# Performance work log

Hardware: AMD Instinct MI355X
Metric: run time of the kernel (lower is better)

The kernel has to match this reference:

```python
import jax, jax.numpy as jnp
from jax import lax
import numpy as np

B, T, C, L, K, LS = 128, 64, 6625, 25, 6, 25
ALPHA, SMOOTH_TAIL, BLANK = 0.1, 0.01, 0


def setup_inputs() -> dict:
    key = jax.random.key(0)
    k1, k2, k3, k4, k5 = jax.random.split(key, 5)
    preds = jax.random.normal(k1, (B, T, C), jnp.float32)
    text = jax.random.randint(k2, (B, L), 1, C)            # labels avoid blank=0
    length = jax.random.randint(k3, (B,), 10, L + 1)       # master target lengths
    preds_size = jnp.full((B,), T, jnp.int32)              # full time length per sample
    smooth_text = jax.random.randint(k4, (B, K, LS), 1, C)
    smooth_length = jax.random.randint(k5, (B, K), 5, LS + 1)
    return dict(preds=preds, text=text, preds_size=preds_size, length=length,
                smooth_text=smooth_text, smooth_length=smooth_length)


def ctc_nll(log_probs, sample_idx, targets, input_lens, target_lens):
    """Batched CTC negative log likelihood (torch.nn.CTCLoss math, zero_infinity).
    log_probs: [T, Bsrc, C] log-softmax; sample_idx: [N] -> Bsrc (lets N targets
    share logits without materializing [T, N, C]); targets: [N, Lmax]."""
    Tt = log_probs.shape[0]
    N, Lt = targets.shape
    S = 2 * Lt + 1
    NEG = jnp.float32(-1e30)
    ext = jnp.full((N, S), BLANK, dtype=targets.dtype).at[:, 1::2].set(targets)
    ext_m2 = jnp.pad(ext[:, :-2], ((0, 0), (2, 0)), constant_values=BLANK)
    allow_skip = (ext != BLANK) & (ext != ext_m2)          # [N, S]

    def frame(lp_t):                                        # [Bsrc,C] -> [N,S]
        return jnp.take_along_axis(lp_t[sample_idx], ext, axis=1)

    lp0 = frame(log_probs[0])
    alpha = jnp.full((N, S), NEG).at[:, 0].set(lp0[:, 0]).at[:, 1].set(lp0[:, 1])

    def step(alpha, xs):
        t, lp_t = xs
        s1 = jnp.pad(alpha[:, :-1], ((0, 0), (1, 0)), constant_values=NEG)
        s2 = jnp.where(allow_skip,
                       jnp.pad(alpha[:, :-2], ((0, 0), (2, 0)), constant_values=NEG), NEG)
        m = jnp.maximum(alpha, jnp.maximum(s1, s2))
        tot = m + jnp.log(jnp.exp(alpha - m) + jnp.exp(s1 - m) + jnp.exp(s2 - m))
        new = tot + frame(lp_t)
        return jnp.where((t < input_lens)[:, None], new, alpha), None

    alpha, _ = lax.scan(step, alpha, (jnp.arange(1, Tt), log_probs[1:]))
    il = (2 * target_lens)[:, None]                         # final blank position
    a_blank = jnp.take_along_axis(alpha, il, axis=1)[:, 0]
    a_char = jnp.take_along_axis(alpha, jnp.maximum(il - 1, 0), axis=1)[:, 0]
    nll = -jnp.logaddexp(a_blank, a_char)
    return jnp.where(nll > 1e29, 0.0, nll)                  # zero_infinity


def _confidence_beam1(lp):
    """CTC prefix beam search with beam_size=1 on one sample. lp: [T, C] log-probs.
    Returns length-normalized prefix probability as the confidence score."""
    Cc = lp.shape[1]
    NEG = jnp.float32(-1e30)
    cs = jnp.arange(Cc)

    def step(state, lp_t):
        lpb, lpnb, last = state
        tot = jnp.logaddexp(lpb, lpnb)
        new_pb = tot + lp_t[BLANK]
        rep = jnp.where(last >= 0, lpnb + lp_t[jnp.maximum(last, 0)], NEG)
        keep = jnp.logaddexp(new_pb, rep)                   # keep same prefix
        ext = jnp.where(cs == last, lpb, tot) + lp_t        # extend by char c
        ext = ext.at[BLANK].set(NEG)
        best_c = jnp.argmax(ext)
        best_ext = ext[best_c]
        take_ext = best_ext > keep
        return (jnp.where(take_ext, NEG, new_pb),
                jnp.where(take_ext, best_ext, rep),
                jnp.where(take_ext, best_c.astype(jnp.int32), last)), None

    init = (jnp.float32(0.0), NEG, jnp.int32(-1))
    (lpb, lpnb, _), _ = lax.scan(step, init, lp)
    score = jnp.logaddexp(lpb, lpnb)
    return jnp.exp(score / lp.shape[0])


def reference(preds, text, preds_size, length, smooth_text, smooth_length):
    lp = jax.nn.log_softmax(preds, axis=2)                  # [B, T, C]
    lp_tbc = jnp.transpose(lp, (1, 0, 2))                   # [T, B, C]
    conf = lax.stop_gradient(jax.vmap(_confidence_beam1)(lp))  # no_grad block

    # master CTC loss (reduction='mean': nll / target_len, then batch mean)
    nll_m = ctc_nll(lp_tbc, jnp.arange(B), text, preds_size, length)
    loss_master = jnp.mean(nll_m / length.astype(lp.dtype))

    # smoothing CTC losses: K hypotheses per sample share that sample's logits
    idx_s = jnp.repeat(jnp.arange(B), K)
    nll_s = ctc_nll(lp_tbc, idx_s, smooth_text.reshape(B * K, LS),
                    jnp.full((B * K,), T, jnp.int32), smooth_length.reshape(B * K))
    loss_cal = jnp.mean((nll_s / smooth_length.reshape(-1).astype(lp.dtype)).reshape(B, K), axis=1)

    ranking = SMOOTH_TAIL + (1.0 - SMOOTH_TAIL) * (1.0 - conf) ** 2
    return loss_master + jnp.mean(ALPHA * ranking * loss_cal)
```

## Files before the change

kernel.cpp:

```cpp
#include <hip/hip_runtime.h>
#include <cstddef>

#define BB   128
#define TT   64
#define CC   6625
#define LL   25
#define KK   6
#define LSS  25
#define SS   51
#define NEG  (-1e30f)
#define FNEG (-3.4e38f)
#define PIVOT 16.0f

#define NCTC       (BB + BB * KK)
#define CTC_BLOCKS (NCTC / 4)

__device__ __forceinline__ float lae(float a, float b) {
    float m = fmaxf(a, b);
    float n = fminf(a, b);
    return m + __logf(1.0f + __expf(n - m));
}

__global__ __launch_bounds__(256) void row_stats_k(
    const float* __restrict__ preds,
    float* __restrict__ lse_t, float* __restrict__ t1v, float* __restrict__ t2v,
    int* __restrict__ t1i, int* __restrict__ t2i, float* __restrict__ cal)
{
    int r = blockIdx.x;
    int tid = threadIdx.x;
    if (r == 0 && tid < BB) cal[tid] = 0.0f;

    const float* row = preds + (size_t)r * CC;
    float s = 0.0f;
    float v1 = FNEG, v2 = FNEG;
    int   i1 = 0x7fffffff, i2 = 0x7fffffff;

    auto upd = [&](float x, int c) {
        s += __expf(x - PIVOT);
        if (c >= 1) {
            if (x > v1)      { v2 = v1; i2 = i1; v1 = x; i1 = c; }
            else if (x > v2) { v2 = x; i2 = c; }
        }
    };

    int h = (4 - (r & 3)) & 3;
    if (tid < h) upd(row[tid], tid);
    const float4* vp = (const float4*)(row + h);
    int nv = (CC - h) >> 2;
    for (int i = tid; i < nv; i += 256) {
        float4 x = vp[i];
        int c = h + (i << 2);
        upd(x.x, c); upd(x.y, c + 1); upd(x.z, c + 2); upd(x.w, c + 3);
    }
    int tail0 = h + (nv << 2);
    if (tid < CC - tail0) upd(row[tail0 + tid], tail0 + tid);

    for (int off = 32; off > 0; off >>= 1) {
        s += __shfl_xor(s, off);
        float w1 = __shfl_xor(v1, off); int j1 = __shfl_xor(i1, off);
        float w2 = __shfl_xor(v2, off); int j2 = __shfl_xor(i2, off);
        bool b1 = (w1 > v1) || (w1 == v1 && j1 < i1);
        if (b1) {
            bool b2 = (v1 > w2) || (v1 == w2 && i1 < j2);
            v2 = b2 ? v1 : w2; i2 = b2 ? i1 : j2;
            v1 = w1; i1 = j1;
        } else {
            bool b2 = (w1 > v2) || (w1 == v2 && j1 < i2);
            if (b2) { v2 = w1; i2 = j1; }
        }
    }

    __shared__ float ss_[4], sv1[4], sv2[4];
    __shared__ int   si1[4], si2[4];
    int wave = tid >> 6, lane = tid & 63;
    if (lane == 0) { ss_[wave] = s; sv1[wave] = v1; si1[wave] = i1; sv2[wave] = v2; si2[wave] = i2; }
    __syncthreads();
    if (tid == 0) {
        for (int w = 1; w < 4; ++w) {
            s += ss_[w];
            float w1 = sv1[w]; int j1 = si1[w]; float w2 = sv2[w]; int j2 = si2[w];
            bool b1 = (w1 > v1) || (w1 == v1 && j1 < i1);
            if (b1) {
                bool b2 = (v1 > w2) || (v1 == w2 && i1 < j2);
                v2 = b2 ? v1 : w2; i2 = b2 ? i1 : j2;
                v1 = w1; i1 = j1;
            } else {
                bool b2 = (w1 > v2) || (w1 == v2 && j1 < i2);
                if (b2) { v2 = w1; i2 = j1; }
            }
        }
        int b = r >> 6, t = r & 63;
        int tr = t * BB + b;
        lse_t[tr] = PIVOT + __logf(s);
        t1v[tr] = v1; t1i[tr] = i1;
        t2v[tr] = v2; t2i[tr] = i2;
    }
}

__global__ __launch_bounds__(256) void ctc_beam_k(
    const float* __restrict__ preds, const float* __restrict__ lse_t,
    const float* __restrict__ t1v, const float* __restrict__ t2v,
    const int* __restrict__ t1i, const int* __restrict__ t2i,
    const int* __restrict__ text, const int* __restrict__ length,
    const int* __restrict__ preds_size,
    const int* __restrict__ smooth_text, const int* __restrict__ smooth_length,
    float* __restrict__ nllm, float* __restrict__ cal, float* __restrict__ ranking)
{
    if (blockIdx.x == CTC_BLOCKS) {
        int b = threadIdx.x;
        if (b >= BB) return;
        const float* pb = preds + (size_t)b * TT * CC;
        float lpb = 0.0f, lpnb = NEG;
        int last = -1;
        float pf0[4];
        #pragma unroll
        for (int i = 0; i < 4; ++i) pf0[i] = pb[(size_t)i * CC];
        float lplast_raw = 0.0f;
        for (int t = 0; t < TT; ++t) {
            int tr = t * BB + b;
            float lse = lse_t[tr];
            float w1 = t1v[tr]; int j1 = t1i[tr];
            float w2 = t2v[tr]; int j2 = t2i[tr];
            float lp0 = pf0[t & 3] - lse;
            if (t + 4 < TT) pf0[t & 3] = pb[(size_t)(t + 4) * CC];
            float lplast = (last >= 0) ? (lplast_raw - lse) : NEG;
            float tot = lae(lpb, lpnb);
            float new_pb = tot + lp0;
            float rep = (last >= 0) ? (lpnb + lplast) : NEG;
            float keep = lae(new_pb, rep);
            float best_ext; int best_c;
            if (j1 == last) {
                float eA = lpb + (w1 - lse);
                float eB = tot + (w2 - lse);
                if (eA > eB || (eA == eB && last < j2)) { best_ext = eA; best_c = last; }
                else                                    { best_ext = eB; best_c = j2; }
            } else {
                best_ext = tot + (w1 - lse);
                best_c = j1;
            }
            bool take = best_ext > keep;
            lpb  = take ? NEG : new_pb;
            lpnb = take ? best_ext : rep;
            last = take ? best_c : last;
            if (t + 1 < TT && last >= 0) lplast_raw = pb[(size_t)(t + 1) * CC + last];
        }
        float score = lae(lpb, lpnb);
        float conf = __expf(score * (1.0f / TT));
        float om = 1.0f - conf;
        ranking[b] = 0.01f + 0.99f * om * om;
        return;
    }

    int wave = threadIdx.x >> 6, lane = threadIdx.x & 63;
    int n = blockIdx.x * 4 + wave;
    if (n >= NCTC) return;
    bool master = n < BB;
    int b, tlen, input_len;
    const int* tgt;
    if (master) {
        b = n; tgt = text + (size_t)n * LL; tlen = length[n]; input_len = preds_size[b];
    } else {
        int ns = n - BB;
        b = ns / KK; tgt = smooth_text + (size_t)ns * LSS; tlen = smooth_length[ns]; input_len = TT;
    }

    int s = lane;
    int ext = 0; bool skipok = false;
    if (s < SS && (s & 1)) {
        int li = (s - 1) >> 1;
        ext = tgt[li];
        skipok = (ext != 0) && (li == 0 || ext != tgt[li - 1]);
    }

    const float* pb = preds + (size_t)b * TT * CC;
    float lse_l = lse_t[lane * BB + b];

    float lse0 = __shfl(lse_l, 0);
    float alpha = NEG;
    if (s < 2) alpha = pb[ext] - lse0;

    float pf[4];
    #pragma unroll
    for (int i = 0; i < 4; ++i) pf[i] = pb[(size_t)(1 + i) * CC + ext];
    for (int t = 1; t < TT; ++t) {
        int slot = (t - 1) & 3;
        float lp = pf[slot] - __shfl(lse_l, t);
        if (t + 4 < TT) pf[slot] = pb[(size_t)(t + 4) * CC + ext];
        float a0 = alpha;
        float a1 = __shfl_up(alpha, 1); a1 = (lane >= 1) ? a1 : NEG;
        float a2 = __shfl_up(alpha, 2); a2 = (lane >= 2 && skipok) ? a2 : NEG;
        float m = fmaxf(a0, fmaxf(a1, a2));
        float tot = m + __logf(__expf(a0 - m) + __expf(a1 - m) + __expf(a2 - m));
        float anew = tot + lp;
        alpha = (t < input_len) ? anew : alpha;
    }

    int il = 2 * tlen;
    float a_bl = __shfl(alpha, il);
    float a_ch = __shfl(alpha, il > 0 ? il - 1 : 0);
    float nll = -lae(a_bl, a_ch);
    if (nll > 1e29f) nll = 0.0f;
    if (lane == 0) {
        float v = nll / (float)tlen;
        if (master) nllm[b] = v;
        else        atomicAdd(&cal[b], v * (1.0f / KK));
    }
}

__global__ __launch_bounds__(128) void final_k(
    const float* __restrict__ nllm, const float* __restrict__ ranking,
    const float* __restrict__ cal, float* __restrict__ out)
{
    int b = threadIdx.x;
    float v = nllm[b] + 0.1f * ranking[b] * cal[b];
    for (int off = 32; off > 0; off >>= 1) v += __shfl_xor(v, off);
    __shared__ float sv[2];
    if ((b & 63) == 0) sv[b >> 6] = v;
    __syncthreads();
    if (b == 0) out[0] = (sv[0] + sv[1]) * (1.0f / BB);
}

extern "C" void kernel_launch(void* const* d_in, const int* in_sizes, int n_in,
                              void* d_out, int out_size, void* d_ws, size_t ws_size,
                              hipStream_t stream)
{
    const float* preds         = (const float*)d_in[0];
    const int*   text          = (const int*)d_in[1];
    const int*   preds_size    = (const int*)d_in[2];
    const int*   length        = (const int*)d_in[3];
    const int*   smooth_text   = (const int*)d_in[4];
    const int*   smooth_length = (const int*)d_in[5];
    float* out = (float*)d_out;

    const int RT = BB * TT;
    float* ws     = (float*)d_ws;
    float* lse_t  = ws;
    float* t1v    = ws + RT;
    float* t2v    = ws + 2 * RT;
    int*   t1i    = (int*)(ws + 3 * RT);
    int*   t2i    = (int*)(ws + 4 * RT);
    float* ranking = ws + 5 * RT;
    float* nllm    = ranking + BB;
    float* cal     = nllm + BB;

    row_stats_k<<<RT, 256, 0, stream>>>(preds, lse_t, t1v, t2v, t1i, t2i, cal);
    ctc_beam_k<<<CTC_BLOCKS + 1, 256, 0, stream>>>(preds, lse_t, t1v, t2v, t1i, t2i,
                                                   text, length, preds_size,
                                                   smooth_text, smooth_length,
                                                   nllm, cal, ranking);
    final_k<<<1, 128, 0, stream>>>(nllm, ranking, cal, out);
}
```

Measured before the change: 394.2 us.

## Assign one wavefront per row in row stats and deepen CTC prefetch

The row statistics kernel now gives each 64-lane wavefront a whole row instead of using a 256-thread block per row. This removes the shared-memory cross-wave reduction and the __syncthreads. The row loop is fully unrolled with five float4 loads in flight, four split exp accumulators, and branchless top-2 updates, and the launch uses a quarter as many blocks with an occupancy hint. The CTC and beam loops deepen their register prefetch of per-timestep logits from 4 to 8 steps, which costs more registers per thread.

```diff
diff --git a/kernel.cpp b/kernel.cpp
--- a/kernel.cpp
+++ b/kernel.cpp
@@ -21,74 +21,89 @@
     return m + __logf(1.0f + __expf(n - m));
 }
 
-__global__ __launch_bounds__(256) void row_stats_k(
+__global__ __launch_bounds__(256, 8) void row_stats_k(
     const float* __restrict__ preds,
     float* __restrict__ lse_t, float* __restrict__ t1v, float* __restrict__ t2v,
     int* __restrict__ t1i, int* __restrict__ t2i, float* __restrict__ cal)
 {
-    int r = blockIdx.x;
-    int tid = threadIdx.x;
-    if (r == 0 && tid < BB) cal[tid] = 0.0f;
-
+    if (blockIdx.x == 0 && threadIdx.x < BB) cal[threadIdx.x] = 0.0f;
+
+    int wave = threadIdx.x >> 6, lane = threadIdx.x & 63;
+    int r = blockIdx.x * 4 + wave;
     const float* row = preds + (size_t)r * CC;
-    float s = 0.0f;
+
+    float s0 = 0.0f, s1 = 0.0f, s2 = 0.0f, s3 = 0.0f;
     float v1 = FNEG, v2 = FNEG;
     int   i1 = 0x7fffffff, i2 = 0x7fffffff;
 
-    auto upd = [&](float x, int c) {
-        s += __expf(x - PIVOT);
-        if (c >= 1) {
-            if (x > v1)      { v2 = v1; i2 = i1; v1 = x; i1 = c; }
-            else if (x > v2) { v2 = x; i2 = c; }
-        }
+    auto top2 = [&](float x, int c) {
+        bool g1 = (x > v1);
+        bool g2 = (x > v2);
+        v2 = g1 ? v1 : (g2 ? x : v2);
+        i2 = g1 ? i1 : (g2 ? c : i2);
+        v1 = g1 ? x : v1;
+        i1 = g1 ? c : i1;
     };
+    auto proc4 = [&](float4 x, int c) {
+        s0 += __expf(x.x - PIVOT);
+        s1 += __expf(x.y - PIVOT);
+        s2 += __expf(x.z - PIVOT);
+        s3 += __expf(x.w - PIVOT);
+        top2((c == 0) ? FNEG : x.x, c);
+        top2(x.y, c + 1);
+        top2(x.z, c + 2);
+        top2(x.w, c + 3);
+    };
 
     int h = (4 - (r & 3)) & 3;
-    if (tid < h) upd(row[tid], tid);
+    if (lane < h) {
+        float x = row[lane];
+        s0 += __expf(x - PIVOT);
+        if (lane > 0) top2(x, lane);
+    }
+
     const float4* vp = (const float4*)(row + h);
     int nv = (CC - h) >> 2;
-    for (int i = tid; i < nv; i += 256) {
-        float4 x = vp[i];
-        int c = h + (i << 2);
-        upd(x.x, c); upd(x.y, c + 1); upd(x.z, c + 2); upd(x.w, c + 3);
-    }
-    int tail0 = h + (nv << 2);
-    if (tid < CC - tail0) upd(row[tail0 + tid], tail0 + tid);
-
+
+    #pragma unroll
+    for (int g = 0; g < 5; ++g) {
+        float4 xr[5];
+        #pragma unroll
+        for (int k = 0; k < 5; ++k) xr[k] = vp[(g * 5 + k) * 64 + lane];
+        #pragma unroll
+        for (int k = 0; k < 5; ++k) {
+            int idx = (g * 5 + k) * 64 + lane;
+            proc4(xr[k], h + idx * 4);
+        }
+    }
+    {
+        int idx = 1600 + lane;
+        if (idx < nv) proc4(vp[idx], h + idx * 4);
+    }
+    {
+        int t0 = h + nv * 4;
+        if (lane < CC - t0) {
+            float x = row[t0 + lane];
+            s0 += __expf(x - PIVOT);
+            top2(x, t0 + lane);
+        }
+    }
+
+    float s = (s0 + s1) + (s2 + s3);
     for (int off = 32; off > 0; off >>= 1) {
         s += __shfl_xor(s, off);
         float w1 = __shfl_xor(v1, off); int j1 = __shfl_xor(i1, off);
         float w2 = __shfl_xor(v2, off); int j2 = __shfl_xor(i2, off);
         bool b1 = (w1 > v1) || (w1 == v1 && j1 < i1);
-        if (b1) {
-            bool b2 = (v1 > w2) || (v1 == w2 && i1 < j2);
-            v2 = b2 ? v1 : w2; i2 = b2 ? i1 : j2;
-            v1 = w1; i1 = j1;
-        } else {
-            bool b2 = (w1 > v2) || (w1 == v2 && j1 < i2);
-            if (b2) { v2 = w1; i2 = j1; }
-        }
-    }
-
-    __shared__ float ss_[4], sv1[4], sv2[4];
-    __shared__ int   si1[4], si2[4];
-    int wave = tid >> 6, lane = tid & 63;
-    if (lane == 0) { ss_[wave] = s; sv1[wave] = v1; si1[wave] = i1; sv2[wave] = v2; si2[wave] = i2; }
-    __syncthreads();
-    if (tid == 0) {
-        for (int w = 1; w < 4; ++w) {
-            s += ss_[w];
-            float w1 = sv1[w]; int j1 = si1[w]; float w2 = sv2[w]; int j2 = si2[w];
-            bool b1 = (w1 > v1) || (w1 == v1 && j1 < i1);
-            if (b1) {
-                bool b2 = (v1 > w2) || (v1 == w2 && i1 < j2);
-                v2 = b2 ? v1 : w2; i2 = b2 ? i1 : j2;
-                v1 = w1; i1 = j1;
-            } else {
-                bool b2 = (w1 > v2) || (w1 == v2 && j1 < i2);
-                if (b2) { v2 = w1; i2 = j1; }
-            }
-        }
+        bool b2a = (v1 > w2) || (v1 == w2 && i1 < j2);
+        bool b2b = (w1 > v2) || (w1 == v2 && j1 < i2);
+        float nv2 = b1 ? (b2a ? v1 : w2) : (b2b ? w1 : v2);
+        int   ni2 = b1 ? (b2a ? i1 : j2) : (b2b ? j1 : i2);
+        v1 = b1 ? w1 : v1; i1 = b1 ? j1 : i1;
+        v2 = nv2; i2 = ni2;
+    }
+
+    if (lane == 0) {
         int b = r >> 6, t = r & 63;
         int tr = t * BB + b;
         lse_t[tr] = PIVOT + __logf(s);
@@ -112,17 +127,17 @@
         const float* pb = preds + (size_t)b * TT * CC;
         float lpb = 0.0f, lpnb = NEG;
         int last = -1;
-        float pf0[4];
+        float pf0[8];
         #pragma unroll
-        for (int i = 0; i < 4; ++i) pf0[i] = pb[(size_t)i * CC];
+        for (int i = 0; i < 8; ++i) pf0[i] = pb[(size_t)i * CC];
         float lplast_raw = 0.0f;
         for (int t = 0; t < TT; ++t) {
             int tr = t * BB + b;
             float lse = lse_t[tr];
             float w1 = t1v[tr]; int j1 = t1i[tr];
             float w2 = t2v[tr]; int j2 = t2i[tr];
-            float lp0 = pf0[t & 3] - lse;
-            if (t + 4 < TT) pf0[t & 3] = pb[(size_t)(t + 4) * CC];
+            float lp0 = pf0[t & 7] - lse;
+            if (t + 8 < TT) pf0[t & 7] = pb[(size_t)(t + 8) * CC];
             float lplast = (last >= 0) ? (lplast_raw - lse) : NEG;
             float tot = lae(lpb, lpnb);
             float new_pb = tot + lp0;
@@ -179,13 +194,13 @@
     float alpha = NEG;
     if (s < 2) alpha = pb[ext] - lse0;
 
-    float pf[4];
+    float pf[8];
     #pragma unroll
-    for (int i = 0; i < 4; ++i) pf[i] = pb[(size_t)(1 + i) * CC + ext];
+    for (int i = 0; i < 8; ++i) pf[i] = pb[(size_t)(1 + i) * CC + ext];
     for (int t = 1; t < TT; ++t) {
-        int slot = (t - 1) & 3;
+        int slot = (t - 1) & 7;
         float lp = pf[slot] - __shfl(lse_l, t);
-        if (t + 4 < TT) pf[slot] = pb[(size_t)(t + 4) * CC + ext];
+        if (t + 8 < TT) pf[slot] = pb[(size_t)(t + 8) * CC + ext];
         float a0 = alpha;
         float a1 = __shfl_up(alpha, 1); a1 = (lane >= 1) ? a1 : NEG;
         float a2 = __shfl_up(alpha, 2); a2 = (lane >= 2 && skipok) ? a2 : NEG;
@@ -243,7 +258,7 @@
     float* nllm    = ranking + BB;
     float* cal     = nllm + BB;
 
-    row_stats_k<<<RT, 256, 0, stream>>>(preds, lse_t, t1v, t2v, t1i, t2i, cal);
+    row_stats_k<<<RT / 4, 256, 0, stream>>>(preds, lse_t, t1v, t2v, t1i, t2i, cal);
     ctc_beam_k<<<CTC_BLOCKS + 1, 256, 0, stream>>>(preds, lse_t, t1v, t2v, t1i, t2i,
                                                    text, length, preds_size,
                                                    smooth_text, smooth_length,
```

Result: faster. 353.3 us (-10.4%).
